# Kernel optimization log

Hardware: AMD Instinct MI355X
Metric: run time of the kernel (lower is better)

The kernel has to match this reference:

```python
import jax, jax.numpy as jnp
import numpy as np

B, C, H, W = 16, 3, 128, 128
PATCH = 8
E = 512          # embedding_dim
NH = 8           # num_heads
P = 64           # proj_dim
HID = 2048       # hidden_dim
L = 6            # num_layers
COND = 3
PH, PW = H // PATCH, W // PATCH
S = PH * PW + 1  # sequence length (patches + cond token)
INV_SQRT_E = 1.0 / np.float32(np.sqrt(E))

_PARAM_SHAPES = {
    'patch_w': (E, C, PATCH, PATCH), 'patch_b': (E,),
    'cond_w1': (COND, E), 'cond_b1': (E,), 'cond_w2': (E, E), 'cond_b2': (E,),
    'pos_embed': (1, S, E),
    'enc_vp': (L, NH, E, P), 'enc_kp': (L, NH, E, P), 'enc_qh': (L, NH, S, S), 'enc_lift': (L, 1, NH * P, E),
    'enc_ln1g': (L, E), 'enc_ln1b': (L, E),
    'enc_w1': (L, E, HID), 'enc_b1': (L, HID), 'enc_w2': (L, HID, E), 'enc_b2': (L, E),
    'enc_ln2g': (L, E), 'enc_ln2b': (L, E),
    'dec_vp': (L, NH, E, P), 'dec_kp': (L, NH, E, P), 'dec_qh': (L, NH, S, S), 'dec_lift': (L, 1, NH * P, E),
    'dec_ln2g': (L, E), 'dec_ln2b': (L, E),
    'dec_w1': (L, E, HID), 'dec_b1': (L, HID), 'dec_w2': (L, HID, E), 'dec_b2': (L, E),
    'dec_ln3g': (L, E), 'dec_ln3b': (L, E),
    'final_g': (E,), 'final_b': (E,),
    'deconv_w': (E, C, PATCH, PATCH), 'deconv_b': (C,),
}


def setup_inputs() -> dict:
    key = jax.random.key(0)
    inp = {
        'x': jax.random.normal(jax.random.fold_in(key, 1000), (B, C, H, W), jnp.float32),
        'y': jax.random.normal(jax.random.fold_in(key, 1001), (B, COND), jnp.float32),
    }
    for i, (name, shp) in enumerate(_PARAM_SHAPES.items()):
        w = 0.02 * jax.random.normal(jax.random.fold_in(key, i), shp, jnp.float32)
        if name.endswith('g'):  # layernorm gains near 1
            w = w + 1.0
        inp[name] = w
    return inp


def _ln(x, g, b, eps=1e-5):
    m = x.mean(-1, keepdims=True)
    v = ((x - m) ** 2).mean(-1, keepdims=True)
    return (x - m) * jax.lax.rsqrt(v + eps) * g + b


def _mhsa(x, vp, kp, qh, lift):
    # x: (B,S,E); vp/kp: (NH,E,P); qh: (NH,S,S); lift: (1, NH*P, E)
    k = jnp.einsum('bse,hep->bhsp', x, kp)
    v = jnp.einsum('bse,hep->bhsp', x, vp)
    qv = jnp.einsum('hst,bhtp->bhsp', qh, v)
    # a_ts = (qh@V) @ K^T, then transpose(-2,-1): a[t,s] = qv[s] . k[t]
    a = jnp.einsum('bhsp,bhtp->bhts', qv, k) * INV_SQRT_E
    a = jax.nn.softmax(a, axis=-1)
    o = jnp.einsum('bhst,bhtp->bhsp', a, v)          # (B,NH,S,P)
    o = o.transpose(0, 2, 1, 3).reshape(x.shape[0], S, NH * P)
    return o @ lift[0]


def _block(z, vp, kp, qh, lift, g1, b1, w1, fb1, w2, fb2, g2, b2):
    z = _ln(z + _mhsa(z, vp, kp, qh, lift), g1, b1)
    h = jax.nn.leaky_relu(z @ w1 + fb1, 0.2) @ w2 + fb2  # dropout = identity (eval)
    return _ln(z + h, g2, b2)


def reference(x, y, patch_w, patch_b, cond_w1, cond_b1, cond_w2, cond_b2, pos_embed,
              enc_vp, enc_kp, enc_qh, enc_lift, enc_ln1g, enc_ln1b,
              enc_w1, enc_b1, enc_w2, enc_b2, enc_ln2g, enc_ln2b,
              dec_vp, dec_kp, dec_qh, dec_lift, dec_ln2g, dec_ln2b,
              dec_w1, dec_b1, dec_w2, dec_b2, dec_ln3g, dec_ln3b,
              final_g, final_b, deconv_w, deconv_b):
    b = x.shape[0]
    # Patching: Conv2d(k=p, s=p) == block-reshape + einsum
    xp = x.reshape(b, C, PH, PATCH, PW, PATCH)
    tok = jnp.einsum('bchpwq,ecpq->bhwe', xp, patch_w).reshape(b, PH * PW, E) + patch_b
    cond = jax.nn.leaky_relu(y @ cond_w1 + cond_b1, 0.2)
    cond = jax.nn.leaky_relu(cond @ cond_w2 + cond_b2, 0.2)
    z = jnp.concatenate([cond[:, None, :], tok], axis=1) + pos_embed
    for i in range(L):
        z = _block(z, enc_vp[i], enc_kp[i], enc_qh[i], enc_lift[i],
                   enc_ln1g[i], enc_ln1b[i], enc_w1[i], enc_b1[i],
                   enc_w2[i], enc_b2[i], enc_ln2g[i], enc_ln2b[i])
    for i in range(L):  # decoder: only mhsa_2 / ln2 / ff / ln3 are used
        z = _block(z, dec_vp[i], dec_kp[i], dec_qh[i], dec_lift[i],
                   dec_ln2g[i], dec_ln2b[i], dec_w1[i], dec_b1[i],
                   dec_w2[i], dec_b2[i], dec_ln3g[i], dec_ln3b[i])
    z = _ln(z[:, 1:], final_g, final_b)               # drop cond token
    g = z.reshape(b, PH, PW, E)                        # (B,E,PH,PW) grid, channels-last form
    out = jnp.einsum('bhwe,ecpq->bchpwq', g, deconv_w).reshape(b, C, H, W)
    return out + deconv_b[None, :, None, None]
```

## Files before the change

kernel.cpp:

```cpp
#include <hip/hip_runtime.h>
#include <stdint.h>
#include <math.h>

#define B_    16
#define C_    3
#define HIMG  128
#define E_    512
#define NH_   8
#define S_    257
#define T_    256
#define MTOK  4096
#define MSEQ  4112
#define HID_  2048
#define SP_   288
#define SLAB  (288*288)
#define PS    2105344L
#define INV_SQRT_E 0.044194173824159216f

typedef __attribute__((ext_vector_type(8))) __bf16 bf16x8;
typedef __attribute__((ext_vector_type(4))) float f32x4;

__device__ __forceinline__ void gload16(const void* g, const void* lds)
{
    __builtin_amdgcn_global_load_lds(
        (const __attribute__((address_space(1))) uint32_t*)(uintptr_t)g,
        (__attribute__((address_space(3))) uint32_t*)(uint32_t)(uintptr_t)lds,
        16, 0, 0);
}

template<int WMW, int WNW, bool LEAKY, bool OUTF32>
__device__ __forceinline__ void gemm_core(
    const __bf16* __restrict__ A, int lda,
    const __bf16* __restrict__ Bt, int ldb,
    void* __restrict__ C, int ldc,
    const float* __restrict__ bias, float scale,
    int M, int N, int K, int tm, int tn)
{
    constexpr int BM  = WMW * 64;
    constexpr int BN  = WNW * 32;
    constexpr int T   = WMW * WNW * 64;
    constexpr int ACH = BM * 4;
    constexpr int BCH = BN * 4;
    constexpr int LPT = ACH / T + BCH / T;
    __shared__ __align__(16) __bf16 sA[4][BM * 32];
    __shared__ __align__(16) __bf16 sB[4][BN * 32];

    const int tid  = threadIdx.x;
    const int lane = tid & 63;
    const int wid  = tid >> 6;
    const int wm   = wid / WNW;
    const int wn   = wid % WNW;
    const int lh   = lane >> 4;
    const int ll   = lane & 15;

    const __bf16* Ab = A + (long)tm * BM * lda;
    const __bf16* Bb = Bt + (long)tn * BN * ldb;

    f32x4 acc[4][2] = {};
    const int nst = K >> 5;

    auto stage = [&](int buf, int k0) {
#pragma unroll
        for (int rr = 0; rr < ACH / T; ++rr) {
            const int L = rr * T + tid;
            const int row = L >> 2;
            const int gch = (L & 3) ^ ((row >> 1) & 3);
            gload16(Ab + (long)row * lda + k0 + gch * 8,
                    (const char*)(&sA[buf][0]) + (rr * T + (wid << 6)) * 16);
        }
#pragma unroll
        for (int rr = 0; rr < BCH / T; ++rr) {
            const int L = rr * T + tid;
            const int row = L >> 2;
            const int gch = (L & 3) ^ ((row >> 1) & 3);
            gload16(Bb + (long)row * ldb + k0 + gch * 8,
                    (const char*)(&sB[buf][0]) + (rr * T + (wid << 6)) * 16);
        }
    };

    const int PF = nst < 3 ? nst : 3;
    for (int s = 0; s < PF; ++s) stage(s & 3, s << 5);

    for (int st = 0; st < nst; ++st) {
        const int rem = nst - 1 - st;
        if (rem >= 2)      asm volatile("s_waitcnt vmcnt(%0)" :: "n"(2 * LPT) : "memory");
        else if (rem == 1) asm volatile("s_waitcnt vmcnt(%0)" :: "n"(LPT) : "memory");
        else               asm volatile("s_waitcnt vmcnt(0)" ::: "memory");
        __builtin_amdgcn_s_barrier();
        __builtin_amdgcn_sched_barrier(0);

        if (st + 3 < nst) stage((st + 3) & 3, (st + 3) << 5);

        const int cur = st & 3;
        bf16x8 afr[4], bfr[2];
#pragma unroll
        for (int i = 0; i < 4; ++i) {
            const int rw = wm * 64 + i * 16 + ll;
            const int c  = lh ^ ((rw >> 1) & 3);
            afr[i] = *reinterpret_cast<const bf16x8*>(&sA[cur][rw * 32 + c * 8]);
        }
#pragma unroll
        for (int j = 0; j < 2; ++j) {
            const int rw = wn * 32 + j * 16 + ll;
            const int c  = lh ^ ((rw >> 1) & 3);
            bfr[j] = *reinterpret_cast<const bf16x8*>(&sB[cur][rw * 32 + c * 8]);
        }
#pragma unroll
        for (int i = 0; i < 4; ++i)
#pragma unroll
            for (int j = 0; j < 2; ++j)
                acc[i][j] = __builtin_amdgcn_mfma_f32_16x16x32_bf16(
                                afr[i], bfr[j], acc[i][j], 0, 0, 0);
    }

#pragma unroll
    for (int i = 0; i < 4; ++i)
#pragma unroll
        for (int ii = 0; ii < 4; ++ii) {
            const int m = tm * BM + wm * 64 + i * 16 + lh * 4 + ii;
            if (m >= M) continue;
#pragma unroll
            for (int j = 0; j < 2; ++j) {
                const int n = tn * BN + wn * 32 + j * 16 + ll;
                if (n >= N) continue;
                float v = acc[i][j][ii] * scale;
                if (bias) v += bias[n];
                if (LEAKY) v = v > 0.f ? v : 0.2f * v;
                if (OUTF32) ((float*)C)[(long)m * ldc + n] = v;
                else        ((__bf16*)C)[(long)m * ldc + n] = (__bf16)v;
            }
        }
}

__device__ __forceinline__ int xcd_swizzle(int wg, int nwg)
{
    const int q = nwg >> 3, r = nwg & 7;
    if (q == 0) return wg;
    const int xcd = wg & 7, off = wg >> 3;
    return (xcd < r ? xcd * (q + 1) : r * (q + 1) + (xcd - r) * q) + off;
}

template<int WMW, int WNW, bool LEAKY, bool OUTF32>
__global__ __launch_bounds__(WMW * WNW * 64) void gemm_k(
    const __bf16* __restrict__ A, int lda, const __bf16* __restrict__ Bt, int ldb,
    void* __restrict__ C, int ldc, const float* __restrict__ bias, float scale,
    int M, int N, int K, int ntn)
{
    const int wg = xcd_swizzle(blockIdx.x, gridDim.x);
    gemm_core<WMW, WNW, LEAKY, OUTF32>(A, lda, Bt, ldb, C, ldc, bias, scale,
                                       M, N, K, wg / ntn, wg % ntn);
}

template<int WMW, int WNW>
__global__ __launch_bounds__(WMW * WNW * 64) void gemm_split_k(
    const __bf16* __restrict__ A, int lda, const __bf16* __restrict__ Bt, int ldb,
    __bf16* __restrict__ P, long pstride, const float* __restrict__ bias,
    int M, int N, int K, int npart, int ntn)
{
    const int part = blockIdx.y;
    const int Kp = K / npart;
    const int wg = xcd_swizzle(blockIdx.x, gridDim.x);
    gemm_core<WMW, WNW, false, false>(A + (long)part * Kp, lda,
                                      Bt + (long)part * Kp, ldb,
                                      P + (long)part * pstride, N,
                                      part == 0 ? bias : nullptr, 1.f,
                                      M, N, Kp, wg / ntn, wg % ntn);
}

__global__ __launch_bounds__(256) void qv_k(const __bf16* __restrict__ qhb,
                                            const __bf16* __restrict__ vT,
                                            __bf16* __restrict__ qvcat)
{
    const int bh = blockIdx.z, b = bh >> 3, h = bh & 7;
    gemm_core<2, 2, false, false>(qhb + (long)h * SLAB, SP_,
                                  vT + (long)bh * 64 * SP_, SP_,
                                  qvcat + (long)b * S_ * E_ + h * 64, E_,
                                  nullptr, 1.f, S_, 64, SP_, blockIdx.x, 0);
}

__global__ __launch_bounds__(256) void scores_k(const __bf16* __restrict__ kvcat,
                                                const __bf16* __restrict__ qvcat,
                                                __bf16* __restrict__ attnb)
{
    const int bh = blockIdx.z, b = bh >> 3, h = bh & 7;
    gemm_core<2, 2, false, false>(kvcat + (long)b * S_ * 1024 + h * 64, 1024,
                                  qvcat + (long)b * S_ * E_ + h * 64, E_,
                                  attnb + (long)bh * SLAB, SP_,
                                  nullptr, INV_SQRT_E, S_, S_, 64,
                                  blockIdx.x, blockIdx.y);
}

__global__ __launch_bounds__(256) void av_k(const __bf16* __restrict__ attnb,
                                            const __bf16* __restrict__ vT,
                                            __bf16* __restrict__ ocat)
{
    const int bh = blockIdx.z, b = bh >> 3, h = bh & 7;
    gemm_core<2, 2, false, false>(attnb + (long)bh * SLAB, SP_,
                                  vT + (long)bh * 64 * SP_, SP_,
                                  ocat + (long)b * S_ * E_ + h * 64, E_,
                                  nullptr, 1.f, S_, 64, SP_, blockIdx.x, 0);
}

__global__ void softmax_kernel(__bf16* __restrict__ attnb)
{
    const int rowid = blockIdx.x * 4 + (threadIdx.x >> 6);
    const int lane  = threadIdx.x & 63;
    const int bh = rowid / S_, s = rowid % S_;
    __bf16* p = attnb + (long)bh * SLAB + (long)s * SP_;
    const float v0 = (float)p[lane],       v1 = (float)p[lane + 64];
    const float v2 = (float)p[lane + 128], v3 = (float)p[lane + 192];
    const float vx = (lane == 0) ? (float)p[256] : -1e30f;
    float m = fmaxf(fmaxf(fmaxf(v0, v1), fmaxf(v2, v3)), vx);
#pragma unroll
    for (int o = 32; o; o >>= 1) m = fmaxf(m, __shfl_xor(m, o));
    const float e0 = __expf(v0 - m), e1 = __expf(v1 - m);
    const float e2 = __expf(v2 - m), e3 = __expf(v3 - m);
    const float ex = (lane == 0) ? __expf(vx - m) : 0.f;
    float su = e0 + e1 + e2 + e3 + ex;
#pragma unroll
    for (int o = 32; o; o >>= 1) su += __shfl_xor(su, o);
    const float inv = 1.f / su;
    p[lane]       = (__bf16)(e0 * inv);
    p[lane + 64]  = (__bf16)(e1 * inv);
    p[lane + 128] = (__bf16)(e2 * inv);
    p[lane + 192] = (__bf16)(e3 * inv);
    if (lane == 0) p[256] = (__bf16)(ex * inv);
    if (lane >= 1 && lane < 32) p[256 + lane] = (__bf16)0.f;
}

__global__ void ln_kernel(const float* __restrict__ x,
                          const __bf16* __restrict__ parts, int nparts, long pstride,
                          const float* __restrict__ g, const float* __restrict__ bb,
                          float* __restrict__ outf, __bf16* __restrict__ outb,
                          int skip_cond, int nrows)
{
    const int row = blockIdx.x * 4 + (threadIdx.x >> 6);
    if (row >= nrows) return;
    const int lane = threadIdx.x & 63;
    const long xrow = skip_cond ? (long)row + (row >> 8) + 1 : (long)row;
    const float4* xr = (const float4*)(x + xrow * E_) + lane * 2;
    const float4 a = xr[0], b4 = xr[1];
    float e[8] = {a.x, a.y, a.z, a.w, b4.x, b4.y, b4.z, b4.w};
    for (int p = 0; p < nparts; ++p) {
        const bf16x8 pv = *reinterpret_cast<const bf16x8*>(
            parts + (long)p * pstride + (long)row * E_ + lane * 8);
#pragma unroll
        for (int i = 0; i < 8; ++i) e[i] += (float)pv[i];
    }
    float s = 0.f;
#pragma unroll
    for (int i = 0; i < 8; ++i) s += e[i];
#pragma unroll
    for (int o = 32; o; o >>= 1) s += __shfl_xor(s, o);
    const float mean = s * (1.f / 512.f);
    float v = 0.f;
#pragma unroll
    for (int i = 0; i < 8; ++i) { e[i] -= mean; v += e[i] * e[i]; }
#pragma unroll
    for (int o = 32; o; o >>= 1) v += __shfl_xor(v, o);
    const float inv = rsqrtf(v * (1.f / 512.f) + 1e-5f);
    const float4* gp = (const float4*)g + lane * 2;
    const float4* bp = (const float4*)bb + lane * 2;
    const float4 g0 = gp[0], g1 = gp[1], bb0 = bp[0], bb1 = bp[1];
    const float gv[8] = {g0.x, g0.y, g0.z, g0.w, g1.x, g1.y, g1.z, g1.w};
    const float bv[8] = {bb0.x, bb0.y, bb0.z, bb0.w, bb1.x, bb1.y, bb1.z, bb1.w};
    float o8[8];
#pragma unroll
    for (int i = 0; i < 8; ++i) o8[i] = e[i] * inv * gv[i] + bv[i];
    if (outf) {
        float4* of = (float4*)(outf + (long)row * E_) + lane * 2;
        of[0] = make_float4(o8[0], o8[1], o8[2], o8[3]);
        of[1] = make_float4(o8[4], o8[5], o8[6], o8[7]);
    }
    if (outb) {
        bf16x8 ov;
#pragma unroll
        for (int i = 0; i < 8; ++i) ov[i] = (__bf16)o8[i];
        *reinterpret_cast<bf16x8*>(outb + (long)row * E_ + lane * 8) = ov;
    }
}

__global__ void conv_straight(const float* __restrict__ in, __bf16* __restrict__ out, long n)
{
    const long i = (long)blockIdx.x * 256 + threadIdx.x;
    if (i < n) out[i] = (__bf16)in[i];
}

__global__ void conv_transpose(const float* __restrict__ in, __bf16* __restrict__ out,
                               int R, int C, long in_bs, long out_bs)
{
    __shared__ float tile[32][33];
    const int bt = blockIdx.z;
    const float* ip = in + (long)bt * in_bs;
    __bf16* op = out + (long)bt * out_bs;
    const int r0 = blockIdx.x * 32, c0 = blockIdx.y * 32;
    const int tx = threadIdx.x & 31, ty = threadIdx.x >> 5;
#pragma unroll
    for (int i = 0; i < 32; i += 8) {
        const int rr = r0 + ty + i, cc = c0 + tx;
        tile[ty + i][tx] = (rr < R && cc < C) ? ip[(long)rr * C + cc] : 0.f;
    }
    __syncthreads();
#pragma unroll
    for (int i = 0; i < 32; i += 8) {
        const int cc = c0 + ty + i, rr = r0 + tx;
        if (cc < C && rr < R) op[(long)cc * R + rr] = (__bf16)tile[tx][ty + i];
    }
}

__global__ void wconv_kernel(const float* __restrict__ kp, const float* __restrict__ vp,
                             const float* __restrict__ lift, const float* __restrict__ w1,
                             const float* __restrict__ w2,
                             __bf16* __restrict__ kvT, __bf16* __restrict__ liftT,
                             __bf16* __restrict__ w1T, __bf16* __restrict__ w2T)
{
    const int j = blockIdx.y;
    const float* src; __bf16* dst; int R, C, nb;
    switch (j) {
        case 0:  src = kp;   dst = kvT;          R = 512;  C = 64;   nb = 8; break;
        case 1:  src = vp;   dst = kvT + 262144; R = 512;  C = 64;   nb = 8; break;
        case 2:  src = lift; dst = liftT;        R = 512;  C = 512;  nb = 1; break;
        case 3:  src = w1;   dst = w1T;          R = 512;  C = 2048; nb = 1; break;
        default: src = w2;   dst = w2T;          R = 2048; C = 512;  nb = 1; break;
    }
    const int tR = R >> 5, tC = C >> 5;
    int t = blockIdx.x;
    if (t >= tR * tC * nb) return;
    const int bt = t / (tR * tC);
    t %= tR * tC;
    const int rt = t / tC, ct = t % tC;
    const long bs = (long)R * C;
    const float* ip = src + (long)bt * bs;
    __bf16* op = dst + (long)bt * bs;
    __shared__ float tile[32][33];
    const int tx = threadIdx.x & 31, ty = threadIdx.x >> 5;
#pragma unroll
    for (int i = 0; i < 32; i += 8)
        tile[ty + i][tx] = ip[(long)(rt * 32 + ty + i) * C + ct * 32 + tx];
    __syncthreads();
#pragma unroll
    for (int i = 0; i < 32; i += 8)
        op[(long)(ct * 32 + ty + i) * R + rt * 32 + tx] = (__bf16)tile[tx][ty + i];
}

__global__ void conv_qh(const float* __restrict__ qh, __bf16* __restrict__ out)
{
    const long n = 8L * SLAB;
    for (long o = (long)blockIdx.x * 256 + threadIdx.x; o < n; o += (long)gridDim.x * 256) {
        const int t = (int)(o % SP_);
        const long rr = o / SP_;
        const int s = (int)(rr % SP_);
        const int h = (int)(rr / SP_);
        float v = 0.f;
        if (s < S_ && t < S_) v = qh[((long)h * S_ + s) * S_ + t];
        out[o] = (__bf16)v;
    }
}

__global__ void vtrans_kernel(const __bf16* __restrict__ kvcat, __bf16* __restrict__ vT)
{
    __shared__ __bf16 tile[32][33];
    const int bh = blockIdx.z, b = bh >> 3, h = bh & 7;
    const int t0 = blockIdx.x * 32, p0 = blockIdx.y * 32;
    const int tx = threadIdx.x & 31, ty = threadIdx.x >> 5;
#pragma unroll
    for (int i = 0; i < 32; i += 8) {
        const int t = t0 + ty + i;
        tile[ty + i][tx] = (t < S_) ?
            kvcat[((long)(b * S_ + t)) * 1024 + 512 + h * 64 + p0 + tx] : (__bf16)0.f;
    }
    __syncthreads();
#pragma unroll
    for (int i = 0; i < 32; i += 8)
        vT[(long)bh * 64 * SP_ + (long)(p0 + ty + i) * SP_ + t0 + tx] = tile[tx][ty + i];
}

__global__ void im2col_kernel(const float* __restrict__ x, __bf16* __restrict__ xcol)
{
    const int idx = blockIdx.x * 256 + threadIdx.x;
    if (idx >= MTOK * 192) return;
    const int m = idx / 192, k = idx % 192;
    const int b = m >> 8, t = m & 255;
    const int ph = t >> 4, pw = t & 15;
    const int c = k >> 6, rr = k & 63;
    const int p = rr >> 3, q = rr & 7;
    xcol[idx] = (__bf16)x[(((long)(b * C_ + c) * HIMG) + ph * 8 + p) * HIMG + pw * 8 + q];
}

__global__ void cond_kernel(const float* __restrict__ y,
                            const float* __restrict__ w1, const float* __restrict__ b1,
                            const float* __restrict__ w2, const float* __restrict__ b2,
                            const float* __restrict__ pos,
                            float* __restrict__ z, __bf16* __restrict__ zb)
{
    __shared__ float c1[512];
    const int b = blockIdx.x;
    const int e = threadIdx.x;
    float v = y[b * 3 + 0] * w1[e] + y[b * 3 + 1] * w1[512 + e]
            + y[b * 3 + 2] * w1[1024 + e] + b1[e];
    v = v > 0.f ? v : 0.2f * v;
    c1[e] = v;
    __syncthreads();
    float acc = b2[e];
    for (int k = 0; k < 512; ++k) acc += c1[k] * w2[k * 512 + e];
    acc = acc > 0.f ? acc : 0.2f * acc;
    const float o = acc + pos[e];
    z[(long)b * S_ * E_ + e] = o;
    zb[(long)b * S_ * E_ + e] = (__bf16)o;
}

__global__ void assemble_kernel(const float* __restrict__ tok,
                                const float* __restrict__ pos,
                                float* __restrict__ z, __bf16* __restrict__ zb)
{
    const int idx = blockIdx.x * 256 + threadIdx.x;
    if (idx >= MTOK * E_) return;
    const int m = idx >> 9;
    const int e = idx & 511;
    const int b = m >> 8, t = m & 255;
    const float o = tok[idx] + pos[(1 + t) * E_ + e];
    const long zi = ((long)b * S_ + 1 + t) * E_ + e;
    z[zi] = o;
    zb[zi] = (__bf16)o;
}

__global__ void scatter_kernel(const float* __restrict__ dtmp,
                               const float* __restrict__ db,
                               float* __restrict__ out)
{
    const int idx = blockIdx.x * 256 + threadIdx.x;
    if (idx >= B_ * C_ * HIMG * HIMG) return;
    const int b  = idx / (C_ * HIMG * HIMG);
    const int rm = idx % (C_ * HIMG * HIMG);
    const int c  = rm / (HIMG * HIMG);
    const int hh = (rm % (HIMG * HIMG)) / HIMG;
    const int ww = rm % HIMG;
    const int ph = hh >> 3, p = hh & 7;
    const int pw = ww >> 3, q = ww & 7;
    out[idx] = dtmp[((long)(b * 256 + ph * 16 + pw)) * 192 + c * 64 + p * 8 + q] + db[c];
}

extern "C" void kernel_launch(void* const* d_in, const int* in_sizes, int n_in,
                              void* d_out, int out_size, void* d_ws, size_t ws_size,
                              hipStream_t stream)
{
    const float* x        = (const float*)d_in[0];
    const float* y        = (const float*)d_in[1];
    const float* patch_w  = (const float*)d_in[2];
    const float* patch_b  = (const float*)d_in[3];
    const float* cond_w1  = (const float*)d_in[4];
    const float* cond_b1  = (const float*)d_in[5];
    const float* cond_w2  = (const float*)d_in[6];
    const float* cond_b2  = (const float*)d_in[7];
    const float* pos      = (const float*)d_in[8];
    const float* enc_vp   = (const float*)d_in[9];
    const float* enc_kp   = (const float*)d_in[10];
    const float* enc_qh   = (const float*)d_in[11];
    const float* enc_lift = (const float*)d_in[12];
    const float* enc_ln1g = (const float*)d_in[13];
    const float* enc_ln1b = (const float*)d_in[14];
    const float* enc_w1   = (const float*)d_in[15];
    const float* enc_b1   = (const float*)d_in[16];
    const float* enc_w2   = (const float*)d_in[17];
    const float* enc_b2   = (const float*)d_in[18];
    const float* enc_ln2g = (const float*)d_in[19];
    const float* enc_ln2b = (const float*)d_in[20];
    const float* dec_vp   = (const float*)d_in[21];
    const float* dec_kp   = (const float*)d_in[22];
    const float* dec_qh   = (const float*)d_in[23];
    const float* dec_lift = (const float*)d_in[24];
    const float* dec_ln2g = (const float*)d_in[25];
    const float* dec_ln2b = (const float*)d_in[26];
    const float* dec_w1   = (const float*)d_in[27];
    const float* dec_b1   = (const float*)d_in[28];
    const float* dec_w2   = (const float*)d_in[29];
    const float* dec_b2   = (const float*)d_in[30];
    const float* dec_ln3g = (const float*)d_in[31];
    const float* dec_ln3b = (const float*)d_in[32];
    const float* final_g  = (const float*)d_in[33];
    const float* final_b  = (const float*)d_in[34];
    const float* deconv_w = (const float*)d_in[35];
    const float* deconv_b = (const float*)d_in[36];
    float* out = (float*)d_out;

    char* wp = (char*)d_ws;
    auto alloc_f32 = [&](long n) { float* p = (float*)wp; wp += ((n * 4 + 63) & ~63LL); return p; };
    auto alloc_bf  = [&](long n) { __bf16* p = (__bf16*)wp; wp += ((n * 2 + 63) & ~63LL); return p; };

    float*  z      = alloc_f32(2105344);
    float*  tok    = alloc_f32(2097152);
    float*  dtmp   = alloc_f32(786432);
    __bf16* zb     = alloc_bf(4352L * 512);
    __bf16* xcolb  = alloc_bf(786432);
    __bf16* kvcat  = alloc_bf(4352L * 1024);
    __bf16* qvcat  = alloc_bf(4352L * 512);
    __bf16* ocat   = alloc_bf(4352L * 512);
    __bf16* vT     = alloc_bf(128L * 64 * SP_);
    __bf16* attnb  = alloc_bf(128L * SLAB + 96L * SP_);
    __bf16* hidden = alloc_bf(4224L * 2048);
    __bf16* gbuf   = alloc_bf(4096L * 512);
    __bf16* pwb    = alloc_bf(512L * 192);
    __bf16* dwTb   = alloc_bf(192L * 512);
    __bf16* kvTb   = alloc_bf(1024L * 512);
    __bf16* liftTb = alloc_bf(262144);
    __bf16* w1Tb   = alloc_bf(1048576);
    __bf16* w2Tb   = alloc_bf(1048576);
    __bf16* qhb    = alloc_bf(8L * SLAB + 96L * SP_);
    (void)ws_size; (void)in_sizes; (void)n_in; (void)out_size;

    const dim3 blk(256);

    conv_straight<<<dim3(384), blk, 0, stream>>>(patch_w, pwb, 98304);
    conv_transpose<<<dim3(16, 6, 1), blk, 0, stream>>>(deconv_w, dwTb, 512, 192, 0, 0);

    im2col_kernel<<<dim3(3072), blk, 0, stream>>>(x, xcolb);
    gemm_k<2, 2, false, true><<<dim3(256), blk, 0, stream>>>(
        xcolb, 192, pwb, 192, tok, 512, patch_b, 1.f, MTOK, 512, 192, 8);
    cond_kernel<<<dim3(B_), dim3(512), 0, stream>>>(y, cond_w1, cond_b1,
                                                    cond_w2, cond_b2, pos, z, zb);
    assemble_kernel<<<dim3(8192), blk, 0, stream>>>(tok, pos, z, zb);

    for (int l = 0; l < 12; ++l) {
        const bool enc = l < 6;
        const int  li  = enc ? l : l - 6;
        const float* vp   = (enc ? enc_vp   : dec_vp)   + (long)li * NH_ * E_ * 64;
        const float* kp   = (enc ? enc_kp   : dec_kp)   + (long)li * NH_ * E_ * 64;
        const float* qh   = (enc ? enc_qh   : dec_qh)   + (long)li * NH_ * S_ * S_;
        const float* lift = (enc ? enc_lift : dec_lift) + (long)li * 512 * 512;
        const float* g1   = (enc ? enc_ln1g : dec_ln2g) + li * E_;
        const float* bb1  = (enc ? enc_ln1b : dec_ln2b) + li * E_;
        const float* w1   = (enc ? enc_w1   : dec_w1)   + (long)li * E_ * HID_;
        const float* fb1  = (enc ? enc_b1   : dec_b1)   + li * HID_;
        const float* w2   = (enc ? enc_w2   : dec_w2)   + (long)li * HID_ * E_;
        const float* fb2  = (enc ? enc_b2   : dec_b2)   + li * E_;
        const float* g2   = (enc ? enc_ln2g : dec_ln3g) + li * E_;
        const float* bb2  = (enc ? enc_ln2b : dec_ln3b) + li * E_;

        wconv_kernel<<<dim3(1024, 5), blk, 0, stream>>>(kp, vp, lift, w1, w2,
                                                        kvTb, liftTb, w1Tb, w2Tb);
        conv_qh<<<dim3(2592), blk, 0, stream>>>(qh, qhb);

        gemm_k<2, 4, false, false><<<dim3(264), dim3(512), 0, stream>>>(
            zb, 512, kvTb, 512, kvcat, 1024, nullptr, 1.f, MSEQ, 1024, 512, 8);
        vtrans_kernel<<<dim3(9, 2, 128), blk, 0, stream>>>(kvcat, vT);
        qv_k<<<dim3(3, 1, 128), blk, 0, stream>>>(qhb, vT, qvcat);
        scores_k<<<dim3(3, 5, 128), blk, 0, stream>>>(kvcat, qvcat, attnb);
        softmax_kernel<<<dim3(8224), blk, 0, stream>>>(attnb);
        av_k<<<dim3(3, 1, 128), blk, 0, stream>>>(attnb, vT, ocat);
        gemm_split_k<2, 2><<<dim3(264, 2), blk, 0, stream>>>(
            ocat, 512, liftTb, 512, attnb, PS, nullptr, MSEQ, 512, 512, 2, 8);
        ln_kernel<<<dim3(1028), blk, 0, stream>>>(z, attnb, 2, PS, g1, bb1,
                                                  z, zb, 0, MSEQ);

        gemm_k<2, 4, true, false><<<dim3(528), dim3(512), 0, stream>>>(
            zb, 512, w1Tb, 512, hidden, 2048, fb1, 1.f, MSEQ, HID_, 512, 16);
        gemm_split_k<2, 2><<<dim3(264, 4), blk, 0, stream>>>(
            hidden, 2048, w2Tb, 2048, attnb, PS, fb2, MSEQ, 512, HID_, 4, 8);
        ln_kernel<<<dim3(1028), blk, 0, stream>>>(z, attnb, 4, PS, g2, bb2,
                                                  z, zb, 0, MSEQ);
    }

    ln_kernel<<<dim3(1024), blk, 0, stream>>>(z, nullptr, 0, 0, final_g, final_b,
                                              nullptr, gbuf, 1, MTOK);
    gemm_k<2, 2, false, true><<<dim3(96), blk, 0, stream>>>(
        gbuf, 512, dwTb, 512, dtmp, 192, nullptr, 1.f, MTOK, 192, 512, 3);
    scatter_kernel<<<dim3(3072), blk, 0, stream>>>(dtmp, deconv_b, out);
}
```

Measured before the change: 1.770 ms.

## Fuse attention into flash-style kernel, hoist qh conversion, retune GEMM tiles

Replaces the separate scores GEMM, softmax pass and AV GEMM with one flash-attention kernel that computes scores, an online softmax and the output per 64-row tile. The full per-head score matrix no longer makes a round trip through global memory. The qh-to-bf16 conversion for all 12 layers is moved to a single launch before the layer loop. The KV and FF1 GEMMs switch to smaller 2x2 wave tiles with twice as many workgroups. The bf16 probabilities in the fused kernel and the extra qh staging buffer add some precision and memory trade-offs.

```diff
diff --git a/kernel.cpp b/kernel.cpp
--- a/kernel.cpp
+++ b/kernel.cpp
@@ -178,54 +178,129 @@
                                   nullptr, 1.f, S_, 64, SP_, blockIdx.x, 0);
 }
 
-__global__ __launch_bounds__(256) void scores_k(const __bf16* __restrict__ kvcat,
-                                                const __bf16* __restrict__ qvcat,
-                                                __bf16* __restrict__ attnb)
-{
-    const int bh = blockIdx.z, b = bh >> 3, h = bh & 7;
-    gemm_core<2, 2, false, false>(kvcat + (long)b * S_ * 1024 + h * 64, 1024,
-                                  qvcat + (long)b * S_ * E_ + h * 64, E_,
-                                  attnb + (long)bh * SLAB, SP_,
-                                  nullptr, INV_SQRT_E, S_, S_, 64,
-                                  blockIdx.x, blockIdx.y);
-}
-
-__global__ __launch_bounds__(256) void av_k(const __bf16* __restrict__ attnb,
+__global__ __launch_bounds__(256) void fa_k(const __bf16* __restrict__ kvcat,
+                                            const __bf16* __restrict__ qvcat,
                                             const __bf16* __restrict__ vT,
                                             __bf16* __restrict__ ocat)
 {
-    const int bh = blockIdx.z, b = bh >> 3, h = bh & 7;
-    gemm_core<2, 2, false, false>(attnb + (long)bh * SLAB, SP_,
-                                  vT + (long)bh * 64 * SP_, SP_,
-                                  ocat + (long)b * S_ * E_ + h * 64, E_,
-                                  nullptr, 1.f, S_, 64, SP_, blockIdx.x, 0);
-}
-
-__global__ void softmax_kernel(__bf16* __restrict__ attnb)
-{
-    const int rowid = blockIdx.x * 4 + (threadIdx.x >> 6);
-    const int lane  = threadIdx.x & 63;
-    const int bh = rowid / S_, s = rowid % S_;
-    __bf16* p = attnb + (long)bh * SLAB + (long)s * SP_;
-    const float v0 = (float)p[lane],       v1 = (float)p[lane + 64];
-    const float v2 = (float)p[lane + 128], v3 = (float)p[lane + 192];
-    const float vx = (lane == 0) ? (float)p[256] : -1e30f;
-    float m = fmaxf(fmaxf(fmaxf(v0, v1), fmaxf(v2, v3)), vx);
-#pragma unroll
-    for (int o = 32; o; o >>= 1) m = fmaxf(m, __shfl_xor(m, o));
-    const float e0 = __expf(v0 - m), e1 = __expf(v1 - m);
-    const float e2 = __expf(v2 - m), e3 = __expf(v3 - m);
-    const float ex = (lane == 0) ? __expf(vx - m) : 0.f;
-    float su = e0 + e1 + e2 + e3 + ex;
-#pragma unroll
-    for (int o = 32; o; o >>= 1) su += __shfl_xor(su, o);
-    const float inv = 1.f / su;
-    p[lane]       = (__bf16)(e0 * inv);
-    p[lane + 64]  = (__bf16)(e1 * inv);
-    p[lane + 128] = (__bf16)(e2 * inv);
-    p[lane + 192] = (__bf16)(e3 * inv);
-    if (lane == 0) p[256] = (__bf16)(ex * inv);
-    if (lane >= 1 && lane < 32) p[256 + lane] = (__bf16)0.f;
+    __shared__ __align__(16) __bf16 sK[64 * 64], sQV[64 * 64], sV[64 * 64];
+    __shared__ __align__(16) __bf16 sP[4][16 * 64];
+    const int bh = blockIdx.y, b = bh >> 3, h = bh & 7;
+    const int i0 = blockIdx.x * 64;
+    const int tid = threadIdx.x, lane = tid & 63, wid = tid >> 6;
+    const int ll = lane & 15, lh = lane >> 4;
+
+    const __bf16* kSrc = kvcat + ((long)(b * S_ + i0)) * 1024 + h * 64;
+    const __bf16* qvB  = qvcat + (long)b * S_ * E_ + h * 64;
+    const __bf16* vTb  = vT + (long)bh * 64 * SP_;
+
+    auto stage64 = [&](__bf16* lds, const __bf16* src, int ldsrc) {
+#pragma unroll
+        for (int r = 0; r < 2; ++r) {
+            const int L = r * 256 + wid * 64 + lane;
+            const int row = L >> 3, c = L & 7;
+            const int sc = c ^ (row & 7);
+            gload16(src + (long)row * ldsrc + sc * 8,
+                    (const char*)lds + (r * 256 + wid * 64) * 16);
+        }
+    };
+
+    stage64(sK, kSrc, 1024);
+    stage64(sQV, qvB, E_);
+    stage64(sV, vTb, SP_);
+    __syncthreads();
+
+    bf16x8 ka[2];
+#pragma unroll
+    for (int ks = 0; ks < 2; ++ks) {
+        const int row = wid * 16 + ll;
+        ka[ks] = *reinterpret_cast<const bf16x8*>(
+            &sK[row * 64 + (((ks * 4 + lh) ^ (row & 7)) << 3)]);
+    }
+
+    float m[4], l[4];
+#pragma unroll
+    for (int ii = 0; ii < 4; ++ii) { m[ii] = -1e30f; l[ii] = 0.f; }
+    f32x4 oacc[4] = {};
+
+    for (int jt = 0; jt < 5; ++jt) {
+        const int j0 = jt * 64;
+        f32x4 s[4] = {};
+#pragma unroll
+        for (int ks = 0; ks < 2; ++ks)
+#pragma unroll
+            for (int nf = 0; nf < 4; ++nf) {
+                const int row = nf * 16 + ll;
+                const bf16x8 qb = *reinterpret_cast<const bf16x8*>(
+                    &sQV[row * 64 + (((ks * 4 + lh) ^ (row & 7)) << 3)]);
+                s[nf] = __builtin_amdgcn_mfma_f32_16x16x32_bf16(ka[ks], qb, s[nf], 0, 0, 0);
+            }
+        float pv[4][4];
+#pragma unroll
+        for (int ii = 0; ii < 4; ++ii) {
+            float mx = -1e30f;
+#pragma unroll
+            for (int nf = 0; nf < 4; ++nf) {
+                float sv = s[nf][ii] * INV_SQRT_E;
+                if (j0 + nf * 16 + ll >= S_) sv = -1e30f;
+                pv[nf][ii] = sv;
+                mx = fmaxf(mx, sv);
+            }
+#pragma unroll
+            for (int msk = 1; msk < 16; msk <<= 1) mx = fmaxf(mx, __shfl_xor(mx, msk));
+            const float mnew = fmaxf(m[ii], mx);
+            const float resc = __expf(m[ii] - mnew);
+            m[ii] = mnew;
+            float sum = 0.f;
+#pragma unroll
+            for (int nf = 0; nf < 4; ++nf) {
+                const float e = __expf(pv[nf][ii] - mnew);
+                pv[nf][ii] = e; sum += e;
+            }
+#pragma unroll
+            for (int msk = 1; msk < 16; msk <<= 1) sum += __shfl_xor(sum, msk);
+            l[ii] = l[ii] * resc + sum;
+#pragma unroll
+            for (int pf = 0; pf < 4; ++pf) oacc[pf][ii] *= resc;
+        }
+        __bf16* sPw = &sP[wid][0];
+#pragma unroll
+        for (int nf = 0; nf < 4; ++nf)
+#pragma unroll
+            for (int ii = 0; ii < 4; ++ii) {
+                const int row = lh * 4 + ii, col = ll + 16 * nf;
+                sPw[row * 64 + ((((col >> 3) ^ (row & 7)) << 3) | (col & 7))] =
+                    (__bf16)pv[nf][ii];
+            }
+#pragma unroll
+        for (int ks = 0; ks < 2; ++ks) {
+            const bf16x8 pa = *reinterpret_cast<const bf16x8*>(
+                &sPw[ll * 64 + (((ks * 4 + lh) ^ (ll & 7)) << 3)]);
+#pragma unroll
+            for (int pf = 0; pf < 4; ++pf) {
+                const int row = pf * 16 + ll;
+                const bf16x8 vb = *reinterpret_cast<const bf16x8*>(
+                    &sV[row * 64 + (((ks * 4 + lh) ^ (row & 7)) << 3)]);
+                oacc[pf] = __builtin_amdgcn_mfma_f32_16x16x32_bf16(pa, vb, oacc[pf], 0, 0, 0);
+            }
+        }
+        if (jt < 4) {
+            __syncthreads();
+            stage64(sQV, qvB + (long)(j0 + 64) * E_, E_);
+            stage64(sV, vTb + j0 + 64, SP_);
+            __syncthreads();
+        }
+    }
+#pragma unroll
+    for (int ii = 0; ii < 4; ++ii) {
+        const int i = i0 + wid * 16 + lh * 4 + ii;
+        if (i >= S_) continue;
+        const float invl = 1.f / l[ii];
+#pragma unroll
+        for (int pf = 0; pf < 4; ++pf)
+            ocat[((long)(b * S_ + i)) * E_ + h * 64 + pf * 16 + ll] =
+                (__bf16)(oacc[pf][ii] * invl);
+    }
 }
 
 __global__ void ln_kernel(const float* __restrict__ x,
@@ -343,16 +418,24 @@
         op[(long)(ct * 32 + ty + i) * R + rt * 32 + tx] = (__bf16)tile[tx][ty + i];
 }
 
-__global__ void conv_qh(const float* __restrict__ qh, __bf16* __restrict__ out)
-{
-    const long n = 8L * SLAB;
+__global__ void conv_qh_all(const float* __restrict__ enc_qh,
+                            const float* __restrict__ dec_qh,
+                            __bf16* __restrict__ out)
+{
+    const long n = 12L * 8 * SLAB;
     for (long o = (long)blockIdx.x * 256 + threadIdx.x; o < n; o += (long)gridDim.x * 256) {
         const int t = (int)(o % SP_);
         const long rr = o / SP_;
         const int s = (int)(rr % SP_);
-        const int h = (int)(rr / SP_);
+        const long hh = rr / SP_;
+        const int h = (int)(hh % 8);
+        const int lyr = (int)(hh / 8);
         float v = 0.f;
-        if (s < S_ && t < S_) v = qh[((long)h * S_ + s) * S_ + t];
+        if (s < S_ && t < S_) {
+            const float* src = (lyr < 6 ? enc_qh + (long)lyr * 8 * S_ * S_
+                                        : dec_qh + (long)(lyr - 6) * 8 * S_ * S_);
+            v = src[((long)h * S_ + s) * S_ + t];
+        }
         out[o] = (__bf16)v;
     }
 }
@@ -496,7 +579,7 @@
     __bf16* qvcat  = alloc_bf(4352L * 512);
     __bf16* ocat   = alloc_bf(4352L * 512);
     __bf16* vT     = alloc_bf(128L * 64 * SP_);
-    __bf16* attnb  = alloc_bf(128L * SLAB + 96L * SP_);
+    __bf16* psl    = alloc_bf(4L * PS);
     __bf16* hidden = alloc_bf(4224L * 2048);
     __bf16* gbuf   = alloc_bf(4096L * 512);
     __bf16* pwb    = alloc_bf(512L * 192);
@@ -505,13 +588,14 @@
     __bf16* liftTb = alloc_bf(262144);
     __bf16* w1Tb   = alloc_bf(1048576);
     __bf16* w2Tb   = alloc_bf(1048576);
-    __bf16* qhb    = alloc_bf(8L * SLAB + 96L * SP_);
+    __bf16* qhb12  = alloc_bf(12L * 8 * SLAB + 96L * SP_);
     (void)ws_size; (void)in_sizes; (void)n_in; (void)out_size;
 
     const dim3 blk(256);
 
     conv_straight<<<dim3(384), blk, 0, stream>>>(patch_w, pwb, 98304);
     conv_transpose<<<dim3(16, 6, 1), blk, 0, stream>>>(deconv_w, dwTb, 512, 192, 0, 0);
+    conv_qh_all<<<dim3(4096), blk, 0, stream>>>(enc_qh, dec_qh, qhb12);
 
     im2col_kernel<<<dim3(3072), blk, 0, stream>>>(x, xcolb);
     gemm_k<2, 2, false, true><<<dim3(256), blk, 0, stream>>>(
@@ -525,7 +609,6 @@
         const int  li  = enc ? l : l - 6;
         const float* vp   = (enc ? enc_vp   : dec_vp)   + (long)li * NH_ * E_ * 64;
         const float* kp   = (enc ? enc_kp   : dec_kp)   + (long)li * NH_ * E_ * 64;
-        const float* qh   = (enc ? enc_qh   : dec_qh)   + (long)li * NH_ * S_ * S_;
         const float* lift = (enc ? enc_lift : dec_lift) + (long)li * 512 * 512;
         const float* g1   = (enc ? enc_ln1g : dec_ln2g) + li * E_;
         const float* bb1  = (enc ? enc_ln1b : dec_ln2b) + li * E_;
@@ -535,28 +618,26 @@
         const float* fb2  = (enc ? enc_b2   : dec_b2)   + li * E_;
         const float* g2   = (enc ? enc_ln2g : dec_ln3g) + li * E_;
         const float* bb2  = (enc ? enc_ln2b : dec_ln3b) + li * E_;
+        const __bf16* qhb = qhb12 + (long)l * 8 * SLAB;
 
         wconv_kernel<<<dim3(1024, 5), blk, 0, stream>>>(kp, vp, lift, w1, w2,
                                                         kvTb, liftTb, w1Tb, w2Tb);
-        conv_qh<<<dim3(2592), blk, 0, stream>>>(qh, qhb);
-
-        gemm_k<2, 4, false, false><<<dim3(264), dim3(512), 0, stream>>>(
-            zb, 512, kvTb, 512, kvcat, 1024, nullptr, 1.f, MSEQ, 1024, 512, 8);
+
+        gemm_k<2, 2, false, false><<<dim3(528), blk, 0, stream>>>(
+            zb, 512, kvTb, 512, kvcat, 1024, nullptr, 1.f, MSEQ, 1024, 512, 16);
         vtrans_kernel<<<dim3(9, 2, 128), blk, 0, stream>>>(kvcat, vT);
         qv_k<<<dim3(3, 1, 128), blk, 0, stream>>>(qhb, vT, qvcat);
-        scores_k<<<dim3(3, 5, 128), blk, 0, stream>>>(kvcat, qvcat, attnb);
-        softmax_kernel<<<dim3(8224), blk, 0, stream>>>(attnb);
-        av_k<<<dim3(3, 1, 128), blk, 0, stream>>>(attnb, vT, ocat);
+        fa_k<<<dim3(5, 128), blk, 0, stream>>>(kvcat, qvcat, vT, ocat);
         gemm_split_k<2, 2><<<dim3(264, 2), blk, 0, stream>>>(
-            ocat, 512, liftTb, 512, attnb, PS, nullptr, MSEQ, 512, 512, 2, 8);
-        ln_kernel<<<dim3(1028), blk, 0, stream>>>(z, attnb, 2, PS, g1, bb1,
+            ocat, 512, liftTb, 512, psl, PS, nullptr, MSEQ, 512, 512, 2, 8);
+        ln_kernel<<<dim3(1028), blk, 0, stream>>>(z, psl, 2, PS, g1, bb1,
                                                   z, zb, 0, MSEQ);
 
-        gemm_k<2, 4, true, false><<<dim3(528), dim3(512), 0, stream>>>(
-            zb, 512, w1Tb, 512, hidden, 2048, fb1, 1.f, MSEQ, HID_, 512, 16);
+        gemm_k<2, 2, true, false><<<dim3(1056), blk, 0, stream>>>(
+            zb, 512, w1Tb, 512, hidden, 2048, fb1, 1.f, MSEQ, HID_, 512, 32);
         gemm_split_k<2, 2><<<dim3(264, 4), blk, 0, stream>>>(
-            hidden, 2048, w2Tb, 2048, attnb, PS, fb2, MSEQ, 512, HID_, 4, 8);
-        ln_kernel<<<dim3(1028), blk, 0, stream>>>(z, attnb, 4, PS, g2, bb2,
+            hidden, 2048, w2Tb, 2048, psl, PS, fb2, MSEQ, 512, HID_, 4, 8);
+        ln_kernel<<<dim3(1028), blk, 0, stream>>>(z, psl, 4, PS, g2, bb2,
                                                   z, zb, 0, MSEQ);
     }
 
```

Result: faster. 1.576 ms (-11.0%).
